# Optimization experiments

Hardware: AMD Instinct MI355X
Metric: run time of the kernel (lower is better)

The kernel has to match this reference:

```python
import jax, jax.numpy as jnp
import numpy as np
import math

D_MODEL = 768
N_HEADS = 12
D_HEAD = D_MODEL // N_HEADS


def setup_inputs() -> dict:
    key = jax.random.key(0)
    ks = jax.random.split(key, 5)
    x = jax.random.normal(ks[0], (2, 4096, D_MODEL), dtype=jnp.float32)
    s = 1.0 / math.sqrt(D_MODEL)
    W_qkv = jax.random.normal(ks[1], (D_MODEL, 3 * D_MODEL), dtype=jnp.float32) * s
    b_qkv = jnp.zeros((3 * D_MODEL,), dtype=jnp.float32)
    W_out = jax.random.normal(ks[2], (D_MODEL, D_MODEL), dtype=jnp.float32) * s
    b_out = jnp.zeros((D_MODEL,), dtype=jnp.float32)
    return {"x": x, "W_qkv": W_qkv, "b_qkv": b_qkv, "W_out": W_out, "b_out": b_out}


def reference(x, W_qkv, b_qkv, W_out, b_out):
    B, T, C = x.shape
    H, Dh = N_HEADS, D_HEAD
    qkv = x @ W_qkv + b_qkv                      # [B,T,3C]
    q, k, v = jnp.split(qkv, 3, axis=-1)
    q = q.reshape(B, T, H, Dh).transpose(0, 2, 1, 3)  # [B,H,T,Dh]
    k = k.reshape(B, T, H, Dh).transpose(0, 2, 1, 3)
    v = v.reshape(B, T, H, Dh).transpose(0, 2, 1, 3)
    att = jnp.einsum('bhqd,bhkd->bhqk', q, k) * (1.0 / math.sqrt(Dh))
    causal = jnp.tril(jnp.ones((T, T), dtype=bool))
    att = jnp.where(causal, att, -jnp.inf)
    att = jax.nn.softmax(att, axis=-1)
    out = jnp.einsum('bhqk,bhkd->bhqd', att, v)  # [B,H,T,Dh]
    out = out.transpose(0, 2, 1, 3).reshape(B, T, C)
    return out @ W_out + b_out
```

## Files before the change

kernel.cpp:

```cpp
#include <hip/hip_runtime.h>
#include <hip/hip_bf16.h>
#include <cstdint>

#define NH 12
#define DH 64
#define TSEQ 4096
#define BATCH 2
#define CDIM 768
#define MROWS (BATCH*TSEQ)

typedef __bf16 bf16x8 __attribute__((ext_vector_type(8)));
typedef __bf16 bf16x4 __attribute__((ext_vector_type(4)));
typedef bf16x8 bf16x8_a __attribute__((may_alias));
typedef bf16x4 bf16x4_a __attribute__((may_alias));
typedef float f32x4 __attribute__((ext_vector_type(4)));
typedef uint32_t u32;

__device__ __forceinline__ uint16_t f2bu(float f) {
  uint32_t u = __float_as_uint(f);
  u += 0x7fffu + ((u >> 16) & 1u);
  return (uint16_t)(u >> 16);
}

__device__ __forceinline__ float bu2f(uint16_t x) {
  return __uint_as_float(((uint32_t)x) << 16);
}

__device__ __forceinline__ u32 pkbf(float a, float b) {
  union { __bf16 h[2]; u32 u; } t;
  t.h[0] = (__bf16)a; t.h[1] = (__bf16)b;
  return t.u;
}

__device__ __forceinline__ bf16x8 mkfrag(u32 a, u32 b, u32 c, u32 d) {
  union { u32 u[4]; bf16x8 v; } t;
  t.u[0] = a; t.u[1] = b; t.u[2] = c; t.u[3] = d;
  return t.v;
}

__device__ __forceinline__ void gload_lds16(const void* g, void* l) {
  __builtin_amdgcn_global_load_lds(
      (const __attribute__((address_space(1))) void*)g,
      (__attribute__((address_space(3))) void*)l, 16, 0, 0);
}

__global__ void cast_f32_bf16(const float* __restrict__ in, uint16_t* __restrict__ out, int n4) {
  int i = blockIdx.x * blockDim.x + threadIdx.x;
  int stride = gridDim.x * blockDim.x;
  for (; i < n4; i += stride) {
    float4 v = ((const float4*)in)[i];
    ushort4 o;
    o.x = f2bu(v.x); o.y = f2bu(v.y); o.z = f2bu(v.z); o.w = f2bu(v.w);
    ((ushort4*)out)[i] = o;
  }
}

__global__ void transpose_cast(const float* __restrict__ w, uint16_t* __restrict__ wt, int K, int N) {
  __shared__ float tile[32][33];
  int kb = blockIdx.x * 32, nb = blockIdx.y * 32;
  int tx = threadIdx.x & 31, ty = threadIdx.x >> 5;
  #pragma unroll
  for (int r = ty; r < 32; r += 8) tile[r][tx] = w[(size_t)(kb + r) * N + nb + tx];
  __syncthreads();
  #pragma unroll
  for (int r = ty; r < 32; r += 8) wt[(size_t)(nb + r) * K + kb + tx] = f2bu(tile[tx][r]);
}

__global__ __launch_bounds__(256) void gemm_qkv(
    const uint16_t* __restrict__ A, const uint16_t* __restrict__ Bt,
    const float* __restrict__ bias,
    uint16_t* __restrict__ q, uint16_t* __restrict__ k, uint16_t* __restrict__ v,
    int N, int K) {
  __shared__ uint16_t As[128 * 32];
  __shared__ uint16_t Bs[128 * 32];
  int tid = threadIdx.x;
  int w = tid >> 6, l = tid & 63;
  int lg = l >> 4, lr = l & 15;
  int mb = blockIdx.x * 128, nb = blockIdx.y * 128;
  int wr = (w >> 1) * 64, wc = (w & 1) * 64;
  f32x4 acc[4][4] = {};
  int srow = tid >> 2, scol = (tid & 3) * 8;
  const uint16_t* Ag = A + (size_t)(mb + srow) * K + scol;
  const uint16_t* Bg = Bt + (size_t)(nb + srow) * K + scol;
  char* AsB = (char*)As + (size_t)w * 1024;
  char* BsB = (char*)Bs + (size_t)w * 1024;
  size_t rowskip = (size_t)64 * K;
  for (int kb = 0; kb < K; kb += 32) {
    __syncthreads();
    gload_lds16(Ag + kb, AsB);
    gload_lds16(Ag + kb + rowskip, AsB + 4096);
    gload_lds16(Bg + kb, BsB);
    gload_lds16(Bg + kb + rowskip, BsB + 4096);
    __syncthreads();
    bf16x8 af[4], bfr[4];
    #pragma unroll
    for (int i = 0; i < 4; ++i)
      af[i] = *(const bf16x8_a*)(const void*)(As + (wr + i * 16 + lr) * 32 + lg * 8);
    #pragma unroll
    for (int i = 0; i < 4; ++i)
      bfr[i] = *(const bf16x8_a*)(const void*)(Bs + (wc + i * 16 + lr) * 32 + lg * 8);
    #pragma unroll
    for (int mi = 0; mi < 4; ++mi)
      #pragma unroll
      for (int ni = 0; ni < 4; ++ni)
        acc[mi][ni] = __builtin_amdgcn_mfma_f32_16x16x32_bf16(af[mi], bfr[ni], acc[mi][ni], 0, 0, 0);
  }
  #pragma unroll
  for (int mi = 0; mi < 4; ++mi) {
    #pragma unroll
    for (int ni = 0; ni < 4; ++ni) {
      int gm0 = mb + wr + mi * 16 + lg * 4;
      int gn = nb + wc + ni * 16 + lr;
      int which = gn / CDIM;
      int cc = gn - which * CDIM;
      int hh = cc >> 6, d = cc & 63;
      float bs = bias[gn];
      if (which == 2) {
        int b0 = gm0 >> 12, t0 = gm0 & 4095;
        ushort4 pk;
        pk.x = f2bu(acc[mi][ni][0] + bs);
        pk.y = f2bu(acc[mi][ni][1] + bs);
        pk.z = f2bu(acc[mi][ni][2] + bs);
        pk.w = f2bu(acc[mi][ni][3] + bs);
        *(ushort4*)&v[(((size_t)(b0 * NH + hh)) * DH + d) * TSEQ + t0] = pk;
      } else {
        uint16_t* dst = which ? k : q;
        float sc = which ? 1.0f : 0.1803368801111204f;
        #pragma unroll
        for (int j = 0; j < 4; ++j) {
          int gm = gm0 + j;
          int bb = gm >> 12, t = gm & 4095;
          float val = (acc[mi][ni][j] + bs) * sc;
          dst[(((size_t)(bb * NH + hh)) * TSEQ + t) * DH + d] = f2bu(val);
        }
      }
    }
  }
}

__global__ __launch_bounds__(256) void gemm_out(
    const uint16_t* __restrict__ A, const uint16_t* __restrict__ Bt,
    const float* __restrict__ bias, float* __restrict__ outf, int N, int K) {
  __shared__ uint16_t As[128 * 32];
  __shared__ uint16_t Bs[64 * 32];
  int tid = threadIdx.x;
  int w = tid >> 6, l = tid & 63;
  int lg = l >> 4, lr = l & 15;
  int mb = blockIdx.x * 128, nb = blockIdx.y * 64;
  int wr = w * 32;
  f32x4 acc[2][4] = {};
  int srow = tid >> 2, scol = (tid & 3) * 8;
  const uint16_t* Ag = A + (size_t)(mb + srow) * K + scol;
  const uint16_t* Bg = Bt + (size_t)(nb + srow) * K + scol;
  char* AsB = (char*)As + (size_t)w * 1024;
  char* BsB = (char*)Bs + (size_t)w * 1024;
  size_t rowskip = (size_t)64 * K;
  for (int kb = 0; kb < K; kb += 32) {
    __syncthreads();
    gload_lds16(Ag + kb, AsB);
    gload_lds16(Ag + kb + rowskip, AsB + 4096);
    gload_lds16(Bg + kb, BsB);
    __syncthreads();
    bf16x8 af[2], bfr[4];
    #pragma unroll
    for (int i = 0; i < 2; ++i)
      af[i] = *(const bf16x8_a*)(const void*)(As + (wr + i * 16 + lr) * 32 + lg * 8);
    #pragma unroll
    for (int i = 0; i < 4; ++i)
      bfr[i] = *(const bf16x8_a*)(const void*)(Bs + (i * 16 + lr) * 32 + lg * 8);
    #pragma unroll
    for (int mi = 0; mi < 2; ++mi)
      #pragma unroll
      for (int ni = 0; ni < 4; ++ni)
        acc[mi][ni] = __builtin_amdgcn_mfma_f32_16x16x32_bf16(af[mi], bfr[ni], acc[mi][ni], 0, 0, 0);
  }
  #pragma unroll
  for (int mi = 0; mi < 2; ++mi) {
    #pragma unroll
    for (int ni = 0; ni < 4; ++ni) {
      #pragma unroll
      for (int j = 0; j < 4; ++j) {
        int gm = mb + wr + mi * 16 + lg * 4 + j;
        int gn = nb + ni * 16 + lr;
        outf[(size_t)gm * N + gn] = acc[mi][ni][j] + bias[gn];
      }
    }
  }
}

__device__ __forceinline__ int lbase_qt(int qt) {
  return (qt < 22) ? (qt - 11) * 2 : 22 + (qt - 22) * 3;
}
__device__ __forceinline__ int ebase_qt(int qt) {
  return (qt < 22) ? (qt - 11) : 11 + (qt - 22) * 2;
}

__global__ __launch_bounds__(256) void attn_part(
    const uint16_t* __restrict__ Q, const uint16_t* __restrict__ K,
    const uint16_t* __restrict__ Vt, uint16_t* __restrict__ O,
    uint16_t* __restrict__ Pbuf, float* __restrict__ Pl) {
  int gid = blockIdx.x;
  int widx = gid / 24, bh = gid - widx * 24;
  int qt, c, nch;
  if (widx < 30) { qt = 31 - widx / 3; c = widx % 3; nch = 3; }
  else if (widx < 52) { int u = widx - 30; qt = 21 - (u >> 1); c = u & 1; nch = 2; }
  else { qt = 62 - widx; c = 0; nch = 1; }
  int ntile = 2 * qt + 2;
  int L = (ntile + nch - 1) / nch;
  int t0 = c * L;
  int t1 = min(ntile - 1, t0 + L - 1);

  int b = bh / NH, hd = bh - b * NH;
  size_t base = (size_t)bh * TSEQ * DH;
  int tid = threadIdx.x, w = tid >> 6, lane = tid & 63;
  int lg = lane >> 4, lr = lane & 15;
  __shared__ __align__(16) uint16_t Ks[64 * 64];
  __shared__ __align__(16) uint16_t Vs[64 * 64];
  int srow = tid >> 3;
  int schunk = (tid & 7) ^ (srow & 7) ^ (((srow >> 3) & 1) << 2);
  const uint16_t* Kg0 = K + base + (size_t)srow * DH + schunk * 8;
  const uint16_t* Vg0 = Vt + base + (size_t)srow * TSEQ + schunk * 8;
  char* KsB = (char*)Ks + w * 1024;
  char* VsB = (char*)Vs + w * 1024;

  int rb = ((lr >> 2) << 3) | (lr & 3);
  int ck0 = lg ^ (lr & 3) ^ (((lr >> 2) & 1) << 2);
  int cv0 = lg ^ (lr & 7) ^ (((lr >> 3) & 1) << 2);

  int qb = qt * 128;
  int qgA = qb + w * 16 + lr;
  int qgB = qgA + 64;
  bf16x8 qA0 = *(const bf16x8_a*)(const void*)(Q + base + (size_t)qgA * DH + lg * 8);
  bf16x8 qA1 = *(const bf16x8_a*)(const void*)(Q + base + (size_t)qgA * DH + 32 + lg * 8);
  bf16x8 qB0 = *(const bf16x8_a*)(const void*)(Q + base + (size_t)qgB * DH + lg * 8);
  bf16x8 qB1 = *(const bf16x8_a*)(const void*)(Q + base + (size_t)qgB * DH + 32 + lg * 8);
  f32x4 oA[4] = {}, oB[4] = {};
  float lA = 0.f, lB = 0.f;
  int lg4 = lg * 4, lg8 = lg * 8;

  for (int t = t0; t <= t1; ++t) {
    __syncthreads();
    {
      const uint16_t* kg_ = Kg0 + (size_t)t * (64 * DH);
      const uint16_t* vg_ = Vg0 + (size_t)t * 64;
      gload_lds16(kg_,           KsB);
      gload_lds16(kg_ + 32 * DH, KsB + 4096);
      gload_lds16(vg_,                     VsB);
      gload_lds16(vg_ + (size_t)32 * TSEQ, VsB + 4096);
    }
    __syncthreads();
    bool doA = (t <= 2 * qt);
    int kb0 = t * 64;
    f32x4 sA[4], sB[4];
    __builtin_amdgcn_s_setprio(1);
    #pragma unroll
    for (int ni = 0; ni < 4; ++ni) {
      int row = rb + ((ni & 1) << 2) + ((ni >> 1) << 5);
      int ch = ck0 ^ ((ni & 1) << 2);
      const char* kbp = (const char*)Ks + row * 128;
      bf16x8 kf0 = *(const bf16x8_a*)(kbp + ch * 16);
      bf16x8 kf1 = *(const bf16x8_a*)(kbp + (ch ^ 4) * 16);
      f32x4 s = {};
      s = __builtin_amdgcn_mfma_f32_16x16x32_bf16(kf0, qB0, s, 0, 0, 0);
      s = __builtin_amdgcn_mfma_f32_16x16x32_bf16(kf1, qB1, s, 0, 0, 0);
      sB[ni] = s;
      if (doA) {
        f32x4 sa = {};
        sa = __builtin_amdgcn_mfma_f32_16x16x32_bf16(kf0, qA0, sa, 0, 0, 0);
        sa = __builtin_amdgcn_mfma_f32_16x16x32_bf16(kf1, qA1, sa, 0, 0, 0);
        sA[ni] = sa;
      }
    }
    __builtin_amdgcn_s_setprio(0);
    bf16x8 pfA0, pfA1;
    if (doA) {
      if (t == 2 * qt) {
        int thr = qgA - kb0 - lg8;
        #pragma unroll
        for (int ni = 0; ni < 4; ++ni) {
          int off = ((ni & 1) << 2) + ((ni >> 1) << 5);
          #pragma unroll
          for (int j = 0; j < 4; ++j)
            sA[ni][j] = (off + j <= thr) ? sA[ni][j] : -1e30f;
        }
      }
      u32 ca[8];
      #pragma unroll
      for (int ni = 0; ni < 4; ++ni) {
        float p0 = __builtin_amdgcn_exp2f(sA[ni][0]);
        float p1 = __builtin_amdgcn_exp2f(sA[ni][1]);
        float p2 = __builtin_amdgcn_exp2f(sA[ni][2]);
        float p3 = __builtin_amdgcn_exp2f(sA[ni][3]);
        lA += (p0 + p1) + (p2 + p3);
        ca[2 * ni] = pkbf(p0, p1);
        ca[2 * ni + 1] = pkbf(p2, p3);
      }
      pfA0 = mkfrag(ca[0], ca[1], ca[2], ca[3]);
      pfA1 = mkfrag(ca[4], ca[5], ca[6], ca[7]);
    }
    bf16x8 pfB0, pfB1;
    {
      if (t == 2 * qt + 1) {
        int thr = qgB - kb0 - lg8;
        #pragma unroll
        for (int ni = 0; ni < 4; ++ni) {
          int off = ((ni & 1) << 2) + ((ni >> 1) << 5);
          #pragma unroll
          for (int j = 0; j < 4; ++j)
            sB[ni][j] = (off + j <= thr) ? sB[ni][j] : -1e30f;
        }
      }
      u32 cb[8];
      #pragma unroll
      for (int ni = 0; ni < 4; ++ni) {
        float p0 = __builtin_amdgcn_exp2f(sB[ni][0]);
        float p1 = __builtin_amdgcn_exp2f(sB[ni][1]);
        float p2 = __builtin_amdgcn_exp2f(sB[ni][2]);
        float p3 = __builtin_amdgcn_exp2f(sB[ni][3]);
        lB += (p0 + p1) + (p2 + p3);
        cb[2 * ni] = pkbf(p0, p1);
        cb[2 * ni + 1] = pkbf(p2, p3);
      }
      pfB0 = mkfrag(cb[0], cb[1], cb[2], cb[3]);
      pfB1 = mkfrag(cb[4], cb[5], cb[6], cb[7]);
    }
    __builtin_amdgcn_s_setprio(1);
    #pragma unroll
    for (int nd = 0; nd < 4; ++nd) {
      const char* vb = (const char*)Vs + (nd * 16 + lr) * 128;
      bf16x8 vf0 = *(const bf16x8_a*)(vb + cv0 * 16);
      bf16x8 vf1 = *(const bf16x8_a*)(vb + (cv0 ^ 4) * 16);
      oB[nd] = __builtin_amdgcn_mfma_f32_16x16x32_bf16(pfB0, vf0, oB[nd], 0, 0, 0);
      oB[nd] = __builtin_amdgcn_mfma_f32_16x16x32_bf16(pfB1, vf1, oB[nd], 0, 0, 0);
      if (doA) {
        oA[nd] = __builtin_amdgcn_mfma_f32_16x16x32_bf16(pfA0, vf0, oA[nd], 0, 0, 0);
        oA[nd] = __builtin_amdgcn_mfma_f32_16x16x32_bf16(pfA1, vf1, oA[nd], 0, 0, 0);
      }
    }
    __builtin_amdgcn_s_setprio(0);
  }

  lA += __shfl_xor(lA, 16, 64); lA += __shfl_xor(lA, 32, 64);
  lB += __shfl_xor(lB, 16, 64); lB += __shfl_xor(lB, 32, 64);
  if (nch == 1) {
    float riA = 1.0f / lA, riB = 1.0f / lB;
    #pragma unroll
    for (int j = 0; j < 4; ++j) {
      float rvA = __shfl(riA, (lane & 48) | (lg4 + j), 64);
      float rvB = __shfl(riB, (lane & 48) | (lg4 + j), 64);
      int tA = qb + w * 16 + lg4 + j;
      size_t pA = (size_t)(b * TSEQ + tA) * CDIM + hd * DH + lr;
      size_t pB = pA + (size_t)64 * CDIM;
      #pragma unroll
      for (int nd = 0; nd < 4; ++nd) {
        O[pA + nd * 16] = f2bu(oA[nd][j] * rvA);
        O[pB + nd * 16] = f2bu(oB[nd][j] * rvB);
      }
    }
  } else {
    float* pl = Pl + (size_t)(bh * 64 + lbase_qt(qt) + c) * 128;
    if (lane < 16) {
      pl[w * 16 + lane] = lA;
      pl[64 + w * 16 + lane] = lB;
    }
    if (c == 0) {
      #pragma unroll
      for (int j = 0; j < 4; ++j) {
        int tA = qb + w * 16 + lg4 + j;
        size_t pA = (size_t)(b * TSEQ + tA) * CDIM + hd * DH + lr;
        size_t pB = pA + (size_t)64 * CDIM;
        #pragma unroll
        for (int nd = 0; nd < 4; ++nd) {
          O[pA + nd * 16] = f2bu(oA[nd][j]);
          O[pB + nd * 16] = f2bu(oB[nd][j]);
        }
      }
    } else {
      uint16_t* Pb = Pbuf + (size_t)(bh * 31 + ebase_qt(qt) + (c - 1)) * 8192;
      #pragma unroll
      for (int j = 0; j < 4; ++j) {
        int qlA = w * 16 + lg4 + j;
        #pragma unroll
        for (int nd = 0; nd < 4; ++nd) {
          Pb[qlA * 64 + nd * 16 + lr] = f2bu(oA[nd][j]);
          Pb[(64 + qlA) * 64 + nd * 16 + lr] = f2bu(oB[nd][j]);
        }
      }
    }
  }
}

__global__ __launch_bounds__(256) void attn_reduce(
    const uint16_t* __restrict__ Pbuf, const float* __restrict__ Pl,
    uint16_t* __restrict__ O) {
  int rid = blockIdx.x;
  int bh = rid / 21, qt = 11 + (rid - bh * 21);
  int nch = (qt >= 22) ? 3 : 2;
  int b = bh / NH, hd = bh - b * NH;
  int tid = threadIdx.x;
  const float* pl = Pl + (size_t)(bh * 64 + lbase_qt(qt)) * 128;
  const uint16_t* pb = Pbuf + (size_t)(bh * 31 + ebase_qt(qt)) * 8192;
  #pragma unroll
  for (int it = 0; it < 8; ++it) {
    int idx = it * 256 + tid;
    int q = idx >> 4, dq = idx & 15;
    float lsum = pl[q] + pl[128 + q];
    if (nch == 3) lsum += pl[256 + q];
    float linv = 1.0f / lsum;
    int t = qt * 128 + q;
    size_t po = (size_t)(b * TSEQ + t) * CDIM + hd * DH + dq * 4;
    ushort4 ov = *(const ushort4*)&O[po];
    ushort4 pv = *(const ushort4*)&pb[q * 64 + dq * 4];
    float s0 = bu2f(ov.x) + bu2f(pv.x);
    float s1 = bu2f(ov.y) + bu2f(pv.y);
    float s2 = bu2f(ov.z) + bu2f(pv.z);
    float s3 = bu2f(ov.w) + bu2f(pv.w);
    if (nch == 3) {
      ushort4 pv2 = *(const ushort4*)&pb[8192 + q * 64 + dq * 4];
      s0 += bu2f(pv2.x); s1 += bu2f(pv2.y); s2 += bu2f(pv2.z); s3 += bu2f(pv2.w);
    }
    ushort4 o;
    o.x = f2bu(s0 * linv); o.y = f2bu(s1 * linv);
    o.z = f2bu(s2 * linv); o.w = f2bu(s3 * linv);
    *(ushort4*)&O[po] = o;
  }
}

extern "C" void kernel_launch(void* const* d_in, const int* in_sizes, int n_in,
                              void* d_out, int out_size, void* d_ws, size_t ws_size,
                              hipStream_t stream) {
  const float* x    = (const float*)d_in[0];
  const float* Wqkv = (const float*)d_in[1];
  const float* bqkv = (const float*)d_in[2];
  const float* Wout = (const float*)d_in[3];
  const float* bout = (const float*)d_in[4];
  float* out = (float*)d_out;
  char* ws = (char*)d_ws;

  uint16_t* Xb    = (uint16_t*)(ws + 0);
  uint16_t* Wqkvt = (uint16_t*)(ws + 12582912);
  uint16_t* Woutt = (uint16_t*)(ws + 16121856);
  uint16_t* Qb    = (uint16_t*)(ws + 17301504);
  uint16_t* Kb    = (uint16_t*)(ws + 29884416);
  uint16_t* Vtb   = (uint16_t*)(ws + 42467328);
  uint16_t* Ob    = (uint16_t*)(ws + 55050240);
  uint16_t* Pbuf  = Xb;
  float*    Pl    = (float*)Wqkvt;

  cast_f32_bf16<<<2048, 256, 0, stream>>>(x, Xb, (MROWS * CDIM) / 4);
  transpose_cast<<<dim3(24, 72), 256, 0, stream>>>(Wqkv, Wqkvt, 768, 2304);
  transpose_cast<<<dim3(24, 24), 256, 0, stream>>>(Wout, Woutt, 768, 768);
  gemm_qkv<<<dim3(64, 18), 256, 0, stream>>>(Xb, Wqkvt, bqkv, Qb, Kb, Vtb, 2304, 768);
  attn_part<<<1512, 256, 0, stream>>>(Qb, Kb, Vtb, Ob, Pbuf, Pl);
  attn_reduce<<<504, 256, 0, stream>>>(Pbuf, Pl, Ob);
  gemm_out<<<dim3(64, 12), 256, 0, stream>>>(Ob, Woutt, bout, out, 768, 768);
}
```

Baseline: 176.9 us.

## Double-buffer K/V tiles in LDS to overlap loads with MFMA compute

The attention kernel now keeps two LDS buffers for the K and V tiles. While the current tile is being computed, it issues the global-to-LDS loads for the next tile, and one barrier per iteration replaces the previous two. The goal is to hide global load latency behind MFMA work. The cost is double the LDS footprint, which may lower occupancy. Correctness also depends on the barrier placement waiting for the async LDS loads to finish (vmcnt).

After: 178.6 us. Within noise of the previous version (+0.9%).

```diff
diff --git a/kernel.cpp b/kernel.cpp
--- a/kernel.cpp
+++ b/kernel.cpp
@@ -214,14 +214,12 @@
   size_t base = (size_t)bh * TSEQ * DH;
   int tid = threadIdx.x, w = tid >> 6, lane = tid & 63;
   int lg = lane >> 4, lr = lane & 15;
-  __shared__ __align__(16) uint16_t Ks[64 * 64];
-  __shared__ __align__(16) uint16_t Vs[64 * 64];
+  __shared__ __align__(16) uint16_t Ks[2][64 * 64];
+  __shared__ __align__(16) uint16_t Vs[2][64 * 64];
   int srow = tid >> 3;
   int schunk = (tid & 7) ^ (srow & 7) ^ (((srow >> 3) & 1) << 2);
   const uint16_t* Kg0 = K + base + (size_t)srow * DH + schunk * 8;
   const uint16_t* Vg0 = Vt + base + (size_t)srow * TSEQ + schunk * 8;
-  char* KsB = (char*)Ks + w * 1024;
-  char* VsB = (char*)Vs + w * 1024;
 
   int rb = ((lr >> 2) << 3) | (lr & 3);
   int ck0 = lg ^ (lr & 3) ^ (((lr >> 2) & 1) << 2);
@@ -238,17 +236,24 @@
   float lA = 0.f, lB = 0.f;
   int lg4 = lg * 4, lg8 = lg * 8;
 
+#define STAGE(bufi, tv) do { \
+    char* kd_ = (char*)Ks[bufi] + w * 1024; \
+    char* vd_ = (char*)Vs[bufi] + w * 1024; \
+    const uint16_t* kg_ = Kg0 + (size_t)(tv) * (64 * DH); \
+    const uint16_t* vg_ = Vg0 + (size_t)(tv) * 64; \
+    gload_lds16(kg_,           kd_); \
+    gload_lds16(kg_ + 32 * DH, kd_ + 4096); \
+    gload_lds16(vg_,                     vd_); \
+    gload_lds16(vg_ + (size_t)32 * TSEQ, vd_ + 4096); \
+  } while (0)
+
+  STAGE(0, t0);
+  __syncthreads();
+  int cur = 0;
   for (int t = t0; t <= t1; ++t) {
-    __syncthreads();
-    {
-      const uint16_t* kg_ = Kg0 + (size_t)t * (64 * DH);
-      const uint16_t* vg_ = Vg0 + (size_t)t * 64;
-      gload_lds16(kg_,           KsB);
-      gload_lds16(kg_ + 32 * DH, KsB + 4096);
-      gload_lds16(vg_,                     VsB);
-      gload_lds16(vg_ + (size_t)32 * TSEQ, VsB + 4096);
-    }
-    __syncthreads();
+    if (t + 1 <= t1) STAGE(cur ^ 1, t + 1);
+    const char* Kc = (const char*)Ks[cur];
+    const char* Vc = (const char*)Vs[cur];
     bool doA = (t <= 2 * qt);
     int kb0 = t * 64;
     f32x4 sA[4], sB[4];
@@ -257,7 +262,7 @@
     for (int ni = 0; ni < 4; ++ni) {
       int row = rb + ((ni & 1) << 2) + ((ni >> 1) << 5);
       int ch = ck0 ^ ((ni & 1) << 2);
-      const char* kbp = (const char*)Ks + row * 128;
+      const char* kbp = Kc + row * 128;
       bf16x8 kf0 = *(const bf16x8_a*)(kbp + ch * 16);
       bf16x8 kf1 = *(const bf16x8_a*)(kbp + (ch ^ 4) * 16);
       f32x4 s = {};
@@ -327,7 +332,7 @@
     __builtin_amdgcn_s_setprio(1);
     #pragma unroll
     for (int nd = 0; nd < 4; ++nd) {
-      const char* vb = (const char*)Vs + (nd * 16 + lr) * 128;
+      const char* vb = Vc + (nd * 16 + lr) * 128;
       bf16x8 vf0 = *(const bf16x8_a*)(vb + cv0 * 16);
       bf16x8 vf1 = *(const bf16x8_a*)(vb + (cv0 ^ 4) * 16);
       oB[nd] = __builtin_amdgcn_mfma_f32_16x16x32_bf16(pfB0, vf0, oB[nd], 0, 0, 0);
@@ -338,7 +343,10 @@
       }
     }
     __builtin_amdgcn_s_setprio(0);
-  }
+    __syncthreads();
+    cur ^= 1;
+  }
+#undef STAGE
 
   lA += __shfl_xor(lA, 16, 64); lA += __shfl_xor(lA, 32, 64);
   lB += __shfl_xor(lB, 16, 64); lB += __shfl_xor(lB, 32, 64);
```
